# Kernel optimization log

Hardware: AMD Instinct MI355X
Metric: run time of the kernel (lower is better)

Reference implementation:

```python
import jax, jax.numpy as jnp
import numpy as np

S, B, HQ, HK, D = 2048, 2, 32, 8, 128


def setup_inputs() -> dict:
    key = jax.random.key(0)
    kq, kk, kv = jax.random.split(key, 3)
    return {
        "query": jax.random.normal(kq, (S, B, HQ, D), dtype=jnp.float32),
        "key": jax.random.normal(kk, (S, B, HK, D), dtype=jnp.float32),
        "value": jax.random.normal(kv, (S, B, HK, D), dtype=jnp.float32),
    }


def reference(query, key, value):
    # s b h d -> b s h d (module's rearrange)
    q = jnp.transpose(query, (1, 0, 2, 3))  # [B,S,HQ,D]
    k = jnp.transpose(key, (1, 0, 2, 3))    # [B,S,HK,D]
    v = jnp.transpose(value, (1, 0, 2, 3))
    n_rep = q.shape[2] // k.shape[2]
    # repeat_kv: GQA expand along head dim (repeat_interleave semantics)
    k = jnp.repeat(k, n_rep, axis=2)  # [B,S,HQ,D]
    v = jnp.repeat(v, n_rep, axis=2)
    scale = q.shape[-1] ** -0.5
    # [B,H,Sq,Sk] scores; causal mask
    scores = jnp.einsum("bqhd,bkhd->bhqk", q, k) * scale
    s = scores.shape[-1]
    causal = jnp.tril(jnp.ones((s, s), dtype=bool))
    scores = jnp.where(causal[None, None], scores, jnp.finfo(scores.dtype).min)
    probs = jax.nn.softmax(scores, axis=-1)
    out = jnp.einsum("bhqk,bkhd->bqhd", probs, v)  # [B,S,H,D]
    # back to Megatron output layout [s, b, h*d]
    out = jnp.transpose(out, (1, 0, 2, 3))
    return out.reshape(out.shape[0], out.shape[1], -1)
```

## Files before the change

kernel.cpp:

```cpp
#include <hip/hip_runtime.h>

#define SLEN 2048
#define NB 2
#define NHQ 32
#define NHK 8
#define DH 128
#define QBLK 128
#define KVBLK 64
#define NT (SLEN / KVBLK)
#define NQT (SLEN / QBLK)
#define TILE_B (KVBLK * DH * 2)

typedef float  f32x4  __attribute__((ext_vector_type(4)));
typedef short  bf16x8 __attribute__((ext_vector_type(8)));

__device__ __forceinline__ unsigned short f2bf(float f) {
  union { float f; unsigned int u; } v; v.f = f;
  return (unsigned short)((v.u + 0x7fffu + ((v.u >> 16) & 1u)) >> 16);
}

__device__ __forceinline__ unsigned int cvtpk(float a, float b) {
  unsigned int r;
  asm("v_cvt_pk_bf16_f32 %0, %1, %2" : "=v"(r) : "v"(a), "v"(b));
  return r;
}

#define GLOAD16(g, l)                                                                   \
  __builtin_amdgcn_global_load_lds(                                                    \
      (const __attribute__((address_space(1))) unsigned int*)(g),                      \
      (__attribute__((address_space(3))) unsigned int*)(l), 16, 0, 0)

__global__ __launch_bounds__(256)
void prep_kv(const float* __restrict__ K, const float* __restrict__ V,
             unsigned short* __restrict__ W) {
  const int tile = blockIdx.x;
  const int bh   = blockIdx.y;
  const int tid  = threadIdx.x;
  const size_t krs = (size_t)NB * NHK * DH;
  const float* kb = K + (size_t)bh * DH + (size_t)tile * KVBLK * krs;
  const float* vb = V + (size_t)bh * DH + (size_t)tile * KVBLK * krs;
  unsigned short* kd = W + ((size_t)bh * NT + tile) * (KVBLK * DH);
  unsigned short* vd = W + (size_t)NB * NHK * NT * (KVBLK * DH)
                         + ((size_t)bh * NT + tile) * (KVBLK * DH);
#pragma unroll
  for (int i = 0; i < 4; ++i) {
    const int cid  = tid + 256 * i;
    const int row  = cid >> 4;
    const int cpos = (cid & 15) << 4;
    const int cb   = cpos ^ ((row & 7) << 4);
    const float* s = kb + (size_t)row * krs + (cb >> 1);
    float4 f0 = *(const float4*)s;
    float4 f1 = *(const float4*)(s + 4);
    bf16x8 a;
    a[0]=(short)f2bf(f0.x); a[1]=(short)f2bf(f0.y); a[2]=(short)f2bf(f0.z); a[3]=(short)f2bf(f0.w);
    a[4]=(short)f2bf(f1.x); a[5]=(short)f2bf(f1.y); a[6]=(short)f2bf(f1.z); a[7]=(short)f2bf(f1.w);
    *(bf16x8*)((char*)kd + row * 256 + cpos) = a;
  }
#pragma unroll
  for (int i = 0; i < 4; ++i) {
    const int cid  = tid + 256 * i;
    const int d    = cid >> 3;
    const int cpos = (cid & 7) << 4;
    const int kb2  = cpos ^ ((d & 7) << 4);
    const int p0   = kb2 >> 1;
    bf16x8 a;
#pragma unroll
    for (int j = 0; j < 8; ++j) {
      const int p  = p0 + j;
      const int kv = (p & 32) | ((p & 4) << 2) | ((p & 24) >> 1) | (p & 3);
      a[j] = (short)f2bf(vb[(size_t)kv * krs + d]);
    }
    *(bf16x8*)((char*)vd + d * 128 + cpos) = a;
  }
}

__global__ __launch_bounds__(256, 3)
void fattn_fwd(const float* __restrict__ Q, const unsigned short* __restrict__ KW,
               const unsigned short* __restrict__ VW, float* __restrict__ O) {
  const int tid  = threadIdx.x;
  const int w    = tid >> 6;
  const int lane = tid & 63;
  const int l15  = lane & 15;
  const int g    = lane >> 4;

  const int wg  = (int)blockIdx.x;
  const int xcd = wg & 7;
  const int c0  = wg >> 3;
  const int bh  = 8 * xcd + (c0 & 7);
  const int qt  = (NQT - 1) - (c0 >> 3);
  const int b   = bh >> 5;
  const int h   = bh & (NHQ - 1);
  const int kh  = h >> 2;

  __shared__ alignas(16) unsigned short Kbuf[2][KVBLK * DH];
  __shared__ alignas(16) unsigned short Vbuf[DH * KVBLK];

  const char* kws = (const char*)(KW + ((size_t)(b * NHK + kh) * NT) * (KVBLK * DH));
  const char* vws = (const char*)(VW + ((size_t)(b * NHK + kh) * NT) * (KVBLK * DH));

  const float sc = 0.08838834764831845f * 1.4426950408889634f;

  const int qs0 = qt * QBLK + 32 * w;
  const int nt  = 2 * qt + 2;

  const int xm    = (l15 & 7) << 4;
  const int koffA = l15 * 256 + ((16 * g) ^ xm);
  const int koffB = koffA ^ 64;
  const char* vbA = (const char*)Vbuf + (l15 * 128 + ((16 * g) ^ xm));
  const char* vbB = (const char*)Vbuf + ((l15 * 128 + ((16 * g) ^ xm)) ^ 64);

  bf16x8 qa[2][4];
#pragma unroll
  for (int u = 0; u < 2; ++u) {
    const float* qp = Q + ((size_t)((qs0 + 16 * u + l15) * NB + b) * NHQ + h) * DH;
#pragma unroll
    for (int s = 0; s < 4; ++s) {
      const float* p = qp + 32 * s + 8 * g;
      float4 f0 = *(const float4*)(p);
      float4 f1 = *(const float4*)(p + 4);
      bf16x8 a;
      a[0]=(short)f2bf(f0.x*sc); a[1]=(short)f2bf(f0.y*sc);
      a[2]=(short)f2bf(f0.z*sc); a[3]=(short)f2bf(f0.w*sc);
      a[4]=(short)f2bf(f1.x*sc); a[5]=(short)f2bf(f1.y*sc);
      a[6]=(short)f2bf(f1.z*sc); a[7]=(short)f2bf(f1.w*sc);
      qa[u][s] = a;
    }
  }

  bf16x8 ones;
#pragma unroll
  for (int i = 0; i < 8; ++i) ones[i] = (short)0x3F80;

  f32x4 o[2][8];
#pragma unroll
  for (int u = 0; u < 2; ++u)
#pragma unroll
    for (int dt = 0; dt < 8; ++dt) o[u][dt] = (f32x4){0.f, 0.f, 0.f, 0.f};
  f32x4 lacc[2] = {(f32x4){0.f,0.f,0.f,0.f}, (f32x4){0.f,0.f,0.f,0.f}};

#pragma unroll
  for (int i = 0; i < 4; ++i) {
    const int off = i * 4096 + w * 1024;
    GLOAD16(kws + off + (lane << 4), (char*)Kbuf[0] + off);
  }

  int cur = 0;
  for (int it = 0; it < nt; ++it) {
    {
      const char* vs = vws + (size_t)it * TILE_B;
#pragma unroll
      for (int i = 0; i < 4; ++i) {
        const int off = i * 4096 + w * 1024;
        GLOAD16(vs + off + (lane << 4), (char*)Vbuf + off);
      }
    }
    if (it + 1 < nt) {
      const char* ks = kws + (size_t)(it + 1) * TILE_B;
#pragma unroll
      for (int i = 0; i < 4; ++i) {
        const int off = i * 4096 + w * 1024;
        GLOAD16(ks + off + (lane << 4), (char*)Kbuf[cur ^ 1] + off);
      }
      asm volatile("s_waitcnt vmcnt(8)" ::: "memory");
    } else {
      asm volatile("s_waitcnt vmcnt(4)" ::: "memory");
    }
    __builtin_amdgcn_s_barrier();
    asm volatile("" ::: "memory");

    const char* kbA = (const char*)Kbuf[cur] + koffA;
    const char* kbB = (const char*)Kbuf[cur] + koffB;
    const int kv0 = it * KVBLK;
    const bool live = (kv0 <= qs0 + 31);

    bf16x8 pav[2][2];
    if (live) {
      f32x4 acc[2][4];
#pragma unroll
      for (int u = 0; u < 2; ++u)
#pragma unroll
        for (int c = 0; c < 4; ++c) acc[u][c] = (f32x4){0.f, 0.f, 0.f, 0.f};
      __builtin_amdgcn_s_setprio(1);
#pragma unroll
      for (int s = 0; s < 4; ++s) {
        const char* kp = (s & 1) ? kbB : kbA;
#pragma unroll
        for (int c = 0; c < 4; ++c) {
          bf16x8 kfr = *(const bf16x8*)(kp + 128 * (s >> 1) + 4096 * c);
          acc[0][c] = __builtin_amdgcn_mfma_f32_16x16x32_bf16(kfr, qa[0][s], acc[0][c], 0, 0, 0);
          acc[1][c] = __builtin_amdgcn_mfma_f32_16x16x32_bf16(kfr, qa[1][s], acc[1][c], 0, 0, 0);
        }
      }
      __builtin_amdgcn_s_setprio(0);

#pragma unroll
      for (int u = 0; u < 2; ++u) {
        const int qs   = qs0 + 16 * u;
        const int qrow = qs + l15;
        const bool domask = (kv0 + KVBLK - 1 > qs);
        float p[4][4];
#pragma unroll
        for (int c = 0; c < 4; ++c)
#pragma unroll
          for (int r = 0; r < 4; ++r) {
            float v = acc[u][c][r];
            if (domask) {
              const int kv = kv0 + 16 * c + 4 * g + r;
              v = (kv > qrow) ? -1e30f : v;
            }
            p[c][r] = exp2f(v);
          }
#pragma unroll
        for (int ks = 0; ks < 2; ++ks) {
          union { unsigned int u32[4]; bf16x8 v; } pu;
          pu.u32[0] = cvtpk(p[2 * ks][0], p[2 * ks][1]);
          pu.u32[1] = cvtpk(p[2 * ks][2], p[2 * ks][3]);
          pu.u32[2] = cvtpk(p[2 * ks + 1][0], p[2 * ks + 1][1]);
          pu.u32[3] = cvtpk(p[2 * ks + 1][2], p[2 * ks + 1][3]);
          pav[u][ks] = pu.v;
        }
      }

      lacc[0] = __builtin_amdgcn_mfma_f32_16x16x32_bf16(ones, pav[0][0], lacc[0], 0, 0, 0);
      lacc[0] = __builtin_amdgcn_mfma_f32_16x16x32_bf16(ones, pav[0][1], lacc[0], 0, 0, 0);
      lacc[1] = __builtin_amdgcn_mfma_f32_16x16x32_bf16(ones, pav[1][0], lacc[1], 0, 0, 0);
      lacc[1] = __builtin_amdgcn_mfma_f32_16x16x32_bf16(ones, pav[1][1], lacc[1], 0, 0, 0);
    }

    if (it + 1 < nt) {
      asm volatile("s_waitcnt vmcnt(4)" ::: "memory");
    } else {
      asm volatile("s_waitcnt vmcnt(0)" ::: "memory");
    }
    __builtin_amdgcn_s_barrier();
    asm volatile("" ::: "memory");

    if (live) {
      __builtin_amdgcn_s_setprio(1);
#pragma unroll
      for (int ks = 0; ks < 2; ++ks) {
        const char* vp = ks ? vbB : vbA;
#pragma unroll
        for (int dt = 0; dt < 8; ++dt) {
          bf16x8 vfr = *(const bf16x8*)(vp + 2048 * dt);
          o[0][dt] = __builtin_amdgcn_mfma_f32_16x16x32_bf16(vfr, pav[0][ks], o[0][dt], 0, 0, 0);
          o[1][dt] = __builtin_amdgcn_mfma_f32_16x16x32_bf16(vfr, pav[1][ks], o[1][dt], 0, 0, 0);
        }
      }
      __builtin_amdgcn_s_setprio(0);
    }

    asm volatile("" ::: "memory");
    __builtin_amdgcn_s_barrier();
    cur ^= 1;
  }

#pragma unroll
  for (int u = 0; u < 2; ++u) {
    const float rl = 1.0f / lacc[u][0];
    const int qrow = qs0 + 16 * u + l15;
    float* ob = O + ((size_t)b * NHQ + h) * DH + (size_t)qrow * (NB * NHQ * DH);
#pragma unroll
    for (int dt = 0; dt < 8; ++dt) {
      float4 st;
      st.x = o[u][dt][0] * rl; st.y = o[u][dt][1] * rl;
      st.z = o[u][dt][2] * rl; st.w = o[u][dt][3] * rl;
      *(float4*)(ob + 16 * dt + 4 * g) = st;
    }
  }
}

extern "C" void kernel_launch(void* const* d_in, const int* in_sizes, int n_in,
                              void* d_out, int out_size, void* d_ws, size_t ws_size,
                              hipStream_t stream) {
  const float* Q = (const float*)d_in[0];
  const float* K = (const float*)d_in[1];
  const float* V = (const float*)d_in[2];
  float* Out = (float*)d_out;
  unsigned short* W = (unsigned short*)d_ws;

  dim3 pgrid(NT, NB * NHK);
  prep_kv<<<pgrid, 256, 0, stream>>>(K, V, W);

  const unsigned short* KW = W;
  const unsigned short* VW = W + (size_t)NB * NHK * NT * (KVBLK * DH);
  fattn_fwd<<<dim3(NQT * NB * NHQ), 256, 0, stream>>>(Q, KW, VW, Out);
}
```

Baseline: 117.8 us.

## Single-buffer K tile to cut LDS and raise occupancy to four blocks

New measurement: 344.5 us. 2.93x slower.

```diff
diff --git a/kernel.cpp b/kernel.cpp
--- a/kernel.cpp
+++ b/kernel.cpp
@@ -74,7 +74,7 @@
   }
 }
 
-__global__ __launch_bounds__(256, 3)
+__global__ __launch_bounds__(256, 4)
 void fattn_fwd(const float* __restrict__ Q, const unsigned short* __restrict__ KW,
                const unsigned short* __restrict__ VW, float* __restrict__ O) {
   const int tid  = threadIdx.x;
@@ -92,7 +92,7 @@
   const int h   = bh & (NHQ - 1);
   const int kh  = h >> 2;
 
-  __shared__ alignas(16) unsigned short Kbuf[2][KVBLK * DH];
+  __shared__ alignas(16) unsigned short Kbuf[KVBLK * DH];
   __shared__ alignas(16) unsigned short Vbuf[DH * KVBLK];
 
   const char* kws = (const char*)(KW + ((size_t)(b * NHK + kh) * NT) * (KVBLK * DH));
@@ -104,8 +104,8 @@
   const int nt  = 2 * qt + 2;
 
   const int xm    = (l15 & 7) << 4;
-  const int koffA = l15 * 256 + ((16 * g) ^ xm);
-  const int koffB = koffA ^ 64;
+  const char* kbA = (const char*)Kbuf + (l15 * 256 + ((16 * g) ^ xm));
+  const char* kbB = (const char*)Kbuf + ((l15 * 256 + ((16 * g) ^ xm)) ^ 64);
   const char* vbA = (const char*)Vbuf + (l15 * 128 + ((16 * g) ^ xm));
   const char* vbB = (const char*)Vbuf + ((l15 * 128 + ((16 * g) ^ xm)) ^ 64);
 
@@ -141,41 +141,24 @@
 #pragma unroll
   for (int i = 0; i < 4; ++i) {
     const int off = i * 4096 + w * 1024;
-    GLOAD16(kws + off + (lane << 4), (char*)Kbuf[0] + off);
-  }
-
-  int cur = 0;
+    GLOAD16(kws + off + (lane << 4), (char*)Kbuf + off);
+  }
+#pragma unroll
+  for (int i = 0; i < 4; ++i) {
+    const int off = i * 4096 + w * 1024;
+    GLOAD16(vws + off + (lane << 4), (char*)Vbuf + off);
+  }
+
   for (int it = 0; it < nt; ++it) {
-    {
-      const char* vs = vws + (size_t)it * TILE_B;
-#pragma unroll
-      for (int i = 0; i < 4; ++i) {
-        const int off = i * 4096 + w * 1024;
-        GLOAD16(vs + off + (lane << 4), (char*)Vbuf + off);
-      }
-    }
-    if (it + 1 < nt) {
-      const char* ks = kws + (size_t)(it + 1) * TILE_B;
-#pragma unroll
-      for (int i = 0; i < 4; ++i) {
-        const int off = i * 4096 + w * 1024;
-        GLOAD16(ks + off + (lane << 4), (char*)Kbuf[cur ^ 1] + off);
-      }
-      asm volatile("s_waitcnt vmcnt(8)" ::: "memory");
-    } else {
-      asm volatile("s_waitcnt vmcnt(4)" ::: "memory");
-    }
-    __builtin_amdgcn_s_barrier();
-    asm volatile("" ::: "memory");
-
-    const char* kbA = (const char*)Kbuf[cur] + koffA;
-    const char* kbB = (const char*)Kbuf[cur] + koffB;
+    asm volatile("s_waitcnt vmcnt(4)" ::: "memory");
+    __builtin_amdgcn_s_barrier();
+    asm volatile("" ::: "memory");
+
     const int kv0 = it * KVBLK;
     const bool live = (kv0 <= qs0 + 31);
 
-    bf16x8 pav[2][2];
+    f32x4 acc[2][4];
     if (live) {
-      f32x4 acc[2][4];
 #pragma unroll
       for (int u = 0; u < 2; ++u)
 #pragma unroll
@@ -192,7 +175,23 @@
         }
       }
       __builtin_amdgcn_s_setprio(0);
-
+    }
+
+    asm volatile("" ::: "memory");
+    __builtin_amdgcn_s_barrier();
+    asm volatile("" ::: "memory");
+
+    if (it + 1 < nt) {
+      const char* ks = kws + (size_t)(it + 1) * TILE_B;
+#pragma unroll
+      for (int i = 0; i < 4; ++i) {
+        const int off = i * 4096 + w * 1024;
+        GLOAD16(ks + off + (lane << 4), (char*)Kbuf + off);
+      }
+    }
+
+    bf16x8 pav[2][2];
+    if (live) {
 #pragma unroll
       for (int u = 0; u < 2; ++u) {
         const int qs   = qs0 + 16 * u;
@@ -252,7 +251,16 @@
 
     asm volatile("" ::: "memory");
     __builtin_amdgcn_s_barrier();
-    cur ^= 1;
+    asm volatile("" ::: "memory");
+
+    if (it + 1 < nt) {
+      const char* vs = vws + (size_t)(it + 1) * TILE_B;
+#pragma unroll
+      for (int i = 0; i < 4; ++i) {
+        const int off = i * 4096 + w * 1024;
+        GLOAD16(vs + off + (lane << 4), (char*)Vbuf + off);
+      }
+    }
   }
 
 #pragma unroll
```
